# Kernel optimization log

Hardware: AMD Instinct MI355X
Metric: run time of the kernel (lower is better)

The kernel has to match this reference:

```python
import jax, jax.numpy as jnp
import numpy as np

NUM_ITERATIONS = 3


def _squash(s):
    # Faithful to the torch code: squash over dim=2 of s_j [B,1,nu,us,1],
    # which is the num_units axis. In our [B, nu, us] layout that is axis=1.
    mag_sq = jnp.sum(s ** 2, axis=1, keepdims=True)  # [B,1,us]
    mag = jnp.sqrt(mag_sq)
    return mag_sq / (1.0 + mag_sq) * (s / mag)


def setup_inputs() -> dict:
    key = jax.random.key(0)
    k1, k2 = jax.random.split(key)
    B, in_units, in_channels, num_units, unit_size = 256, 8, 1152, 10, 16
    x = jax.random.normal(k1, (B, in_units, in_channels), dtype=jnp.float32)
    W = jax.random.normal(k2, (1, in_channels, num_units, unit_size, in_units), dtype=jnp.float32)
    return {"x": x, "W": W}


def reference(x, W):
    B = x.shape[0]
    W0 = W[0]  # [ic, nu, us, iu]
    ic, nu = W0.shape[0], W0.shape[1]
    xt = jnp.swapaxes(x, 1, 2)  # [B, ic, iu]
    # u_hat = W @ x per (batch, in_channel, out_unit): [B, ic, nu, us]
    u_hat = jnp.einsum('cdui,bci->bcdu', W0, xt)
    b_ij = jnp.zeros((ic, nu), dtype=x.dtype)
    v = None
    for _ in range(NUM_ITERATIONS):
        c_ij = jax.nn.softmax(b_ij, axis=0)              # softmax over in_channels
        s_j = jnp.einsum('cd,bcdu->bdu', c_ij, u_hat)    # [B, nu, us]
        v = _squash(s_j)                                 # [B, nu, us]
        # agreement: <u_hat, v> over unit_size, mean over batch -> [ic, nu]
        agree = jnp.einsum('bcdu,bdu->cd', u_hat, v) / B
        b_ij = b_ij + agree
    return v  # [B, num_units, unit_size]
```

## Files before the change

### kernel.cpp

```cpp
#include <hip/hip_runtime.h>
#include <math.h>

#define B_  256
#define IU  8
#define IC  1152
#define NU  10
#define US  16
#define CCH 9
#define NCH 128
#define BT  64
#define NBLK 512
#define XSP 516
#define SPSTRIDE ((size_t)NCH * B_ * NU * US)

__device__ __forceinline__ float gld(const float* p) {
    return __hip_atomic_load(p, __ATOMIC_RELAXED, __HIP_MEMORY_SCOPE_AGENT);
}
__device__ __forceinline__ void gst(float* p, float v) {
    __hip_atomic_store(p, v, __ATOMIC_RELAXED, __HIP_MEMORY_SCOPE_AGENT);
}
__device__ __forceinline__ unsigned uld(const unsigned* p) {
    return __hip_atomic_load(p, __ATOMIC_RELAXED, __HIP_MEMORY_SCOPE_AGENT);
}
__device__ __forceinline__ void ust(unsigned* p, unsigned v) {
    __hip_atomic_store(p, v, __ATOMIC_RELAXED, __HIP_MEMORY_SCOPE_AGENT);
}

__device__ __forceinline__ void gridbar(unsigned* bar) {
    __syncthreads();
    if (threadIdx.x == 0) {
        const int bid = blockIdx.x;
        const int leaf = bid >> 3;
        const int mid  = bid >> 6;
        unsigned* myR1 = bar + (96 + leaf) * 32;
        unsigned g = uld(myR1);
        unsigned a = __hip_atomic_fetch_add(bar + leaf * 32, 1u,
                                            __ATOMIC_RELAXED, __HIP_MEMORY_SCOPE_AGENT);
        if (a == 7u) {
            ust(bar + leaf * 32, 0u);
            unsigned b2 = __hip_atomic_fetch_add(bar + (64 + mid) * 32, 1u,
                                                 __ATOMIC_RELAXED, __HIP_MEMORY_SCOPE_AGENT);
            if (b2 == 7u) {
                ust(bar + (64 + mid) * 32, 0u);
                unsigned c2 = __hip_atomic_fetch_add(bar + 72 * 32, 1u,
                                                     __ATOMIC_RELAXED, __HIP_MEMORY_SCOPE_AGENT);
                if (c2 == 7u) {
                    ust(bar + 72 * 32, 0u);
#pragma unroll
                    for (int k = 0; k < 8; k++)
                        ust(bar + (80 + k) * 32, g + 1u);
                }
                while (uld(bar + (80 + mid) * 32) == g)
                    __builtin_amdgcn_s_sleep(8);
#pragma unroll
                for (int j = 0; j < 8; j++)
                    ust(bar + (96 + mid * 8 + j) * 32, g + 1u);
            }
        }
        while (uld(myR1) == g)
            __builtin_amdgcn_s_sleep(16);
    }
    __syncthreads();
}

__global__ __launch_bounds__(256, 2) void mega(const float* __restrict__ x,
                                               const float* __restrict__ W,
                                               float* __restrict__ sp,
                                               float* __restrict__ vb0,
                                               float* __restrict__ vb1,
                                               float* __restrict__ bij,
                                               float* __restrict__ out,
                                               unsigned* __restrict__ bar) {
    __shared__ float4 ws[CCH * NU * 2 * 16];
    __shared__ __align__(16) float xs[CCH * XSP];
    __shared__ float aux[NU * US];
    __shared__ float cs[NU * CCH];

    const int tid = threadIdx.x;
    const int bid = blockIdx.x;
    const int grp = bid & 7;
    const int slot_ = bid >> 3;
    const int ch = ((slot_ >> 2) << 3) | grp;
    const int bt = slot_ & 3;
    const int b0 = bt * BT, c0 = ch * CCH;

    const float4* wg = (const float4*)W + (size_t)c0 * 320;
    for (int q = tid; q < CCH * NU * 32; q += 256) {
        int h = q & 1, u = (q >> 1) & 15, cd = q >> 5;
        ws[(cd * 2 + h) * 16 + u] = wg[q];
    }
    for (int idx = tid; idx < CCH * BT * IU; idx += 256) {
        int cc = idx % CCH;
        int r = idx / CCH;
        xs[cc * XSP + r] = x[((size_t)(b0 + (r >> 3)) * IU + (r & 7)) * IC + c0 + cc];
    }

    const int uq = tid & 15;
    const int bs = tid >> 4;
    const int wv = tid >> 6;
    const int lane = tid & 63;

    for (int iter = 0; iter < 3; ++iter) {
        float* spb = sp + (size_t)iter * SPSTRIDE;

        __syncthreads();
        if (iter == 0) {
            for (int q = tid; q < NU * CCH; q += 256) cs[q] = 1.0f;
        } else {
            for (int d = wv; d < NU; d += 4) {
                const float* brow = bij + (size_t)d * IC;
                float bv[18];
                float mx = -1e30f;
#pragma unroll
                for (int j = 0; j < 18; j++) {
                    bv[j] = gld(brow + lane + j * 64);
                    mx = fmaxf(mx, bv[j]);
                }
#pragma unroll
                for (int off = 32; off > 0; off >>= 1)
                    mx = fmaxf(mx, __shfl_xor(mx, off, 64));
                float sume = 0.0f;
#pragma unroll
                for (int j = 0; j < 18; j++) sume += expf(bv[j] - mx);
#pragma unroll
                for (int off = 32; off > 0; off >>= 1)
                    sume += __shfl_xor(sume, off, 64);
                const float inv = 1.0f / sume;
                if (lane < CCH)
                    cs[d * CCH + lane] = expf(gld(brow + c0 + lane) - mx) * inv;
            }
        }
        __syncthreads();
        const float scale = iter ? 1.0f : (1.0f / (float)IC);

        {
            float acc[4][NU];
#pragma unroll
            for (int bb = 0; bb < 4; bb++)
#pragma unroll
                for (int d = 0; d < NU; d++) acc[bb][d] = 0.0f;

#pragma unroll 3
            for (int cc = 0; cc < CCH; cc++) {
                float4 xv0[4], xv1[4];
#pragma unroll
                for (int bb = 0; bb < 4; bb++) {
                    const float4* xp = (const float4*)(xs + cc * XSP + (bs + 16 * bb) * IU);
                    xv0[bb] = xp[0]; xv1[bb] = xp[1];
                }
#pragma unroll
                for (int d = 0; d < NU; d++) {
                    float4 w0 = ws[((cc * NU + d) * 2 + 0) * 16 + uq];
                    float4 w1 = ws[((cc * NU + d) * 2 + 1) * 16 + uq];
                    const float cw = cs[d * CCH + cc];
#pragma unroll
                    for (int bb = 0; bb < 4; bb++) {
                        float uh = w0.x * xv0[bb].x + w0.y * xv0[bb].y + w0.z * xv0[bb].z + w0.w * xv0[bb].w
                                 + w1.x * xv1[bb].x + w1.y * xv1[bb].y + w1.z * xv1[bb].z + w1.w * xv1[bb].w;
                        acc[bb][d] = fmaf(cw, uh, acc[bb][d]);
                    }
                }
            }
#pragma unroll
            for (int bb = 0; bb < 4; bb++) {
                const int b = b0 + bs + 16 * bb;
#pragma unroll
                for (int d = 0; d < NU; d++)
                    gst(spb + (((size_t)ch * B_ + b) * NU + d) * US + uq, acc[bb][d] * scale);
            }
        }
        gridbar(bar);

        {
            const int batch = bid >> 1;
            const int uh2 = bid & 1;
            if (tid < 160) {
                const int part = tid & 7;
                const int sl20 = tid >> 3;
                const int dL = sl20 >> 1;
                const int pr = sl20 & 1;
                const int sl = dL * 4 + uh2 * 2 + pr;
                const float4* s4p = (const float4*)spb;
                float4 a = make_float4(0.f, 0.f, 0.f, 0.f);
#pragma unroll 4
                for (int m = 0; m < 16; ++m) {
                    float4 t = s4p[((size_t)(part + 8 * m) * B_ + batch) * 40 + sl];
                    a.x += t.x; a.y += t.y; a.z += t.z; a.w += t.w;
                }
                a.x += __shfl_xor(a.x, 1, 64); a.y += __shfl_xor(a.y, 1, 64);
                a.z += __shfl_xor(a.z, 1, 64); a.w += __shfl_xor(a.w, 1, 64);
                a.x += __shfl_xor(a.x, 2, 64); a.y += __shfl_xor(a.y, 2, 64);
                a.z += __shfl_xor(a.z, 2, 64); a.w += __shfl_xor(a.w, 2, 64);
                a.x += __shfl_xor(a.x, 4, 64); a.y += __shfl_xor(a.y, 4, 64);
                a.z += __shfl_xor(a.z, 4, 64); a.w += __shfl_xor(a.w, 4, 64);
                if (part == 0) {
                    aux[dL * 8 + pr * 4 + 0] = a.x;
                    aux[dL * 8 + pr * 4 + 1] = a.y;
                    aux[dL * 8 + pr * 4 + 2] = a.z;
                    aux[dL * 8 + pr * 4 + 3] = a.w;
                }
            }
            __syncthreads();
            if (tid < NU * 8) {
                const int dL = tid >> 3, j = tid & 7;
                float s = aux[dL * 8 + j];
                float msq = 0.0f;
#pragma unroll
                for (int dd = 0; dd < NU; dd++) {
                    float t = aux[dd * 8 + j];
                    msq = fmaf(t, t, msq);
                }
                float f = msq / ((1.0f + msq) * sqrtf(msq));
                const size_t o = (size_t)batch * (NU * US) + dL * US + uh2 * 8 + j;
                if (iter == 2)
                    out[o] = s * f;
                else {
                    float* vdst = (iter == 0) ? vb0 : vb1;
                    gst(vdst + o, s * f);
                }
            }
        }
        if (iter == 2) return;
        gridbar(bar);

        {
            const int cl = tid >> 4;
            const float* vb = (iter == 0) ? vb0 : vb1;
            if (cl < CCH) {
                float4 wA[NU], wB[NU];
#pragma unroll
                for (int d = 0; d < NU; d++) {
                    wA[d] = ws[((cl * NU + d) * 2 + 0) * 16 + uq];
                    wB[d] = ws[((cl * NU + d) * 2 + 1) * 16 + uq];
                }
                float accd[NU];
#pragma unroll
                for (int d = 0; d < NU; d++) accd[d] = 0.0f;
                const int bstag = (cl & 3) * 7;
#pragma unroll 4
                for (int blx = 0; blx < BT; blx++) {
                    const int bl = (blx + bstag) & 63;
                    const float* xp = xs + cl * XSP + bl * IU;
                    float4 x0 = *(const float4*)xp;
                    float4 x1 = *(const float4*)(xp + 4);
                    const float* vp = vb + (size_t)(b0 + bl) * (NU * US) + uq;
#pragma unroll
                    for (int d = 0; d < NU; d++) {
                        float uh = wA[d].x * x0.x + wA[d].y * x0.y + wA[d].z * x0.z + wA[d].w * x0.w
                                 + wB[d].x * x1.x + wB[d].y * x1.y + wB[d].z * x1.z + wB[d].w * x1.w;
                        accd[d] = fmaf(uh, vp[d * US], accd[d]);
                    }
                }
#pragma unroll
                for (int d = 0; d < NU; d++) {
                    float a = accd[d];
                    a += __shfl_xor(a, 1, 64);
                    a += __shfl_xor(a, 2, 64);
                    a += __shfl_xor(a, 4, 64);
                    a += __shfl_xor(a, 8, 64);
                    if (uq == 0)
                        atomicAdd(bij + (size_t)d * IC + c0 + cl, a * (1.0f / (float)B_));
                }
            }
        }
        gridbar(bar);
    }
}

extern "C" void kernel_launch(void* const* d_in, const int* in_sizes, int n_in,
                              void* d_out, int out_size, void* d_ws, size_t ws_size,
                              hipStream_t stream) {
    (void)in_sizes; (void)n_in; (void)out_size; (void)ws_size;
    const float* x = (const float*)d_in[0];
    const float* W = (const float*)d_in[1];
    float* out = (float*)d_out;

    unsigned* bar = (unsigned*)d_ws;
    float* bij = (float*)d_ws + 5120;
    float* sp  = bij + (size_t)NU * IC;
    float* vb0 = sp + 3 * SPSTRIDE;
    float* vb1 = vb0 + (size_t)B_ * NU * US;

    hipMemsetAsync(d_ws, 0, 5120 * 4 + (size_t)NU * IC * 4, stream);
    mega<<<NBLK, 256, 0, stream>>>(x, W, sp, vb0, vb1, bij, out, bar);
}
```

Before: 199.2 us.

## Precompute softmax denominators via last-block tickets and pad partial-sum layout

Removes the per-block full softmax over all 1152 b_ij entries per unit. Instead, the last of the four batch-tile blocks for each channel chunk, detected with an atomic ticket, sums exp(b_ij) for its channels and atomically adds the result into a global esum. Later iterations then read that denominator directly. The max subtraction is dropped, which risks overflow if b_ij grows large. The partial-sum buffer is also relaid out as 192-float rows split by unit-size half, so the reduction phase reads contiguous float4s.

```diff
diff --git a/kernel.cpp b/kernel.cpp
--- a/kernel.cpp
+++ b/kernel.cpp
@@ -11,7 +11,8 @@
 #define BT  64
 #define NBLK 512
 #define XSP 516
-#define SPSTRIDE ((size_t)NCH * B_ * NU * US)
+#define SPROW 192
+#define SPSTRIDE ((size_t)NCH * B_ * SPROW)
 
 __device__ __forceinline__ float gld(const float* p) {
     return __hip_atomic_load(p, __ATOMIC_RELAXED, __HIP_MEMORY_SCOPE_AGENT);
@@ -69,12 +70,15 @@
                                                float* __restrict__ vb0,
                                                float* __restrict__ vb1,
                                                float* __restrict__ bij,
+                                               float* __restrict__ esum,
+                                               unsigned* __restrict__ ticket,
                                                float* __restrict__ out,
                                                unsigned* __restrict__ bar) {
     __shared__ float4 ws[CCH * NU * 2 * 16];
     __shared__ __align__(16) float xs[CCH * XSP];
-    __shared__ float aux[NU * US];
+    __shared__ float aux[NU * 8];
     __shared__ float cs[NU * CCH];
+    __shared__ int lastflag;
 
     const int tid = threadIdx.x;
     const int bid = blockIdx.x;
@@ -97,8 +101,7 @@
 
     const int uq = tid & 15;
     const int bs = tid >> 4;
-    const int wv = tid >> 6;
-    const int lane = tid & 63;
+    const int uh = uq >> 3, uj = uq & 7;
 
     for (int iter = 0; iter < 3; ++iter) {
         float* spb = sp + (size_t)iter * SPSTRIDE;
@@ -107,27 +110,10 @@
         if (iter == 0) {
             for (int q = tid; q < NU * CCH; q += 256) cs[q] = 1.0f;
         } else {
-            for (int d = wv; d < NU; d += 4) {
-                const float* brow = bij + (size_t)d * IC;
-                float bv[18];
-                float mx = -1e30f;
-#pragma unroll
-                for (int j = 0; j < 18; j++) {
-                    bv[j] = gld(brow + lane + j * 64);
-                    mx = fmaxf(mx, bv[j]);
-                }
-#pragma unroll
-                for (int off = 32; off > 0; off >>= 1)
-                    mx = fmaxf(mx, __shfl_xor(mx, off, 64));
-                float sume = 0.0f;
-#pragma unroll
-                for (int j = 0; j < 18; j++) sume += expf(bv[j] - mx);
-#pragma unroll
-                for (int off = 32; off > 0; off >>= 1)
-                    sume += __shfl_xor(sume, off, 64);
-                const float inv = 1.0f / sume;
-                if (lane < CCH)
-                    cs[d * CCH + lane] = expf(gld(brow + c0 + lane) - mx) * inv;
+            for (int q = tid; q < NU * CCH; q += 256) {
+                int d = q / CCH, cc = q - d * CCH;
+                float es = gld(esum + (iter - 1) * 16 + d);
+                cs[q] = expf(gld(bij + (size_t)d * IC + c0 + cc)) / es;
             }
         }
         __syncthreads();
@@ -155,18 +141,19 @@
                     const float cw = cs[d * CCH + cc];
 #pragma unroll
                     for (int bb = 0; bb < 4; bb++) {
-                        float uh = w0.x * xv0[bb].x + w0.y * xv0[bb].y + w0.z * xv0[bb].z + w0.w * xv0[bb].w
-                                 + w1.x * xv1[bb].x + w1.y * xv1[bb].y + w1.z * xv1[bb].z + w1.w * xv1[bb].w;
-                        acc[bb][d] = fmaf(cw, uh, acc[bb][d]);
+                        float uh_ = w0.x * xv0[bb].x + w0.y * xv0[bb].y + w0.z * xv0[bb].z + w0.w * xv0[bb].w
+                                  + w1.x * xv1[bb].x + w1.y * xv1[bb].y + w1.z * xv1[bb].z + w1.w * xv1[bb].w;
+                        acc[bb][d] = fmaf(cw, uh_, acc[bb][d]);
                     }
                 }
             }
 #pragma unroll
             for (int bb = 0; bb < 4; bb++) {
                 const int b = b0 + bs + 16 * bb;
+                float* rowp = spb + ((size_t)ch * B_ + b) * SPROW + uh * 96 + uj;
 #pragma unroll
                 for (int d = 0; d < NU; d++)
-                    gst(spb + (((size_t)ch * B_ + b) * NU + d) * US + uq, acc[bb][d] * scale);
+                    gst(rowp + d * 8, acc[bb][d] * scale);
             }
         }
         gridbar(bar);
@@ -176,15 +163,13 @@
             const int uh2 = bid & 1;
             if (tid < 160) {
                 const int part = tid & 7;
-                const int sl20 = tid >> 3;
-                const int dL = sl20 >> 1;
-                const int pr = sl20 & 1;
-                const int sl = dL * 4 + uh2 * 2 + pr;
+                const int sl = tid >> 3;
                 const float4* s4p = (const float4*)spb;
                 float4 a = make_float4(0.f, 0.f, 0.f, 0.f);
-#pragma unroll 4
+#pragma unroll
                 for (int m = 0; m < 16; ++m) {
-                    float4 t = s4p[((size_t)(part + 8 * m) * B_ + batch) * 40 + sl];
+                    float4 t = s4p[((size_t)(part + 8 * m) * B_ + batch) * (SPROW / 4)
+                                   + uh2 * 24 + sl];
                     a.x += t.x; a.y += t.y; a.z += t.z; a.w += t.w;
                 }
                 a.x += __shfl_xor(a.x, 1, 64); a.y += __shfl_xor(a.y, 1, 64);
@@ -194,16 +179,14 @@
                 a.x += __shfl_xor(a.x, 4, 64); a.y += __shfl_xor(a.y, 4, 64);
                 a.z += __shfl_xor(a.z, 4, 64); a.w += __shfl_xor(a.w, 4, 64);
                 if (part == 0) {
-                    aux[dL * 8 + pr * 4 + 0] = a.x;
-                    aux[dL * 8 + pr * 4 + 1] = a.y;
-                    aux[dL * 8 + pr * 4 + 2] = a.z;
-                    aux[dL * 8 + pr * 4 + 3] = a.w;
+                    aux[sl * 4 + 0] = a.x; aux[sl * 4 + 1] = a.y;
+                    aux[sl * 4 + 2] = a.z; aux[sl * 4 + 3] = a.w;
                 }
             }
             __syncthreads();
             if (tid < NU * 8) {
                 const int dL = tid >> 3, j = tid & 7;
-                float s = aux[dL * 8 + j];
+                float s = aux[tid];
                 float msq = 0.0f;
 #pragma unroll
                 for (int dd = 0; dd < NU; dd++) {
@@ -212,12 +195,8 @@
                 }
                 float f = msq / ((1.0f + msq) * sqrtf(msq));
                 const size_t o = (size_t)batch * (NU * US) + dL * US + uh2 * 8 + j;
-                if (iter == 2)
-                    out[o] = s * f;
-                else {
-                    float* vdst = (iter == 0) ? vb0 : vb1;
-                    gst(vdst + o, s * f);
-                }
+                if (iter == 2) gst(out + o, s * f);
+                else           gst(((iter == 0) ? vb0 : vb1) + o, s * f);
             }
         }
         if (iter == 2) return;
@@ -246,9 +225,9 @@
                     const float* vp = vb + (size_t)(b0 + bl) * (NU * US) + uq;
 #pragma unroll
                     for (int d = 0; d < NU; d++) {
-                        float uh = wA[d].x * x0.x + wA[d].y * x0.y + wA[d].z * x0.z + wA[d].w * x0.w
-                                 + wB[d].x * x1.x + wB[d].y * x1.y + wB[d].z * x1.z + wB[d].w * x1.w;
-                        accd[d] = fmaf(uh, vp[d * US], accd[d]);
+                        float uh_ = wA[d].x * x0.x + wA[d].y * x0.y + wA[d].z * x0.z + wA[d].w * x0.w
+                                  + wB[d].x * x1.x + wB[d].y * x1.y + wB[d].z * x1.z + wB[d].w * x1.w;
+                        accd[d] = fmaf(uh_, vp[d * US], accd[d]);
                     }
                 }
 #pragma unroll
@@ -262,6 +241,21 @@
                         atomicAdd(bij + (size_t)d * IC + c0 + cl, a * (1.0f / (float)B_));
                 }
             }
+            __syncthreads();
+            if (tid == 0) {
+                unsigned old = __hip_atomic_fetch_add(ticket + iter * 128 + ch, 1u,
+                                                      __ATOMIC_RELAXED,
+                                                      __HIP_MEMORY_SCOPE_AGENT);
+                lastflag = (old == 3u);
+            }
+            __syncthreads();
+            if (lastflag && tid < NU) {
+                float es = 0.0f;
+#pragma unroll
+                for (int cc = 0; cc < CCH; cc++)
+                    es += expf(gld(bij + (size_t)tid * IC + c0 + cc));
+                atomicAdd(esum + iter * 16 + tid, es);
+            }
         }
         gridbar(bar);
     }
@@ -276,11 +270,13 @@
     float* out = (float*)d_out;
 
     unsigned* bar = (unsigned*)d_ws;
-    float* bij = (float*)d_ws + 5120;
+    unsigned* ticket = bar + 5120;
+    float* esum = (float*)(ticket + 256);
+    float* bij = esum + 32;
     float* sp  = bij + (size_t)NU * IC;
     float* vb0 = sp + 3 * SPSTRIDE;
     float* vb1 = vb0 + (size_t)B_ * NU * US;
 
-    hipMemsetAsync(d_ws, 0, 5120 * 4 + (size_t)NU * IC * 4, stream);
-    mega<<<NBLK, 256, 0, stream>>>(x, W, sp, vb0, vb1, bij, out, bar);
-}
+    hipMemsetAsync(d_ws, 0, (5120 + 256) * 4 + 32 * 4 + (size_t)NU * IC * 4, stream);
+    mega<<<NBLK, 256, 0, stream>>>(x, W, sp, vb0, vb1, bij, esum, ticket, out, bar);
+}
```

Result: no change. 200.7 us (+0.7%).
